# Kernel tuning notes

Hardware: AMD Instinct MI355X
Metric: run time of the kernel (lower is better)

The kernel has to match this reference:

```python
import jax, jax.numpy as jnp
import numpy as np

HID = 1024
HEADS = 16
HEAD_DIM = HID // HEADS
SCALE = np.sqrt(HEAD_DIM).astype(np.float32)


def setup_inputs() -> dict:
    key = jax.random.key(0)
    ks = jax.random.split(key, 13)
    B, S = 4, 2048
    inp = {
        'query': jax.random.normal(ks[0], (B, S, HID), jnp.float32),
        'key': jax.random.normal(ks[1], (B, S, HID), jnp.float32),
        'value': jax.random.normal(ks[2], (B, S, HID), jnp.float32),
        'mask': jax.random.randint(ks[3], (B, 1, 1, S), 0, 2, jnp.int32),
        'Wq': jax.random.normal(ks[4], (HID, HID), jnp.float32) / np.sqrt(HID),
        'bq': jax.random.normal(ks[5], (HID,), jnp.float32) * 0.02,
        'Wk': jax.random.normal(ks[6], (HID, HID), jnp.float32) / np.sqrt(HID),
        'bk': jax.random.normal(ks[7], (HID,), jnp.float32) * 0.02,
        'Wv': jax.random.normal(ks[8], (HID, HID), jnp.float32) / np.sqrt(HID),
        'bv': jax.random.normal(ks[9], (HID,), jnp.float32) * 0.02,
        'Wo': jax.random.normal(ks[10], (HID, HID), jnp.float32) / np.sqrt(HID),
        'bo': jax.random.normal(ks[11], (HID,), jnp.float32) * 0.02,
    }
    return inp


def reference(query, key, value, mask, Wq, bq, Wk, bk, Wv, bv, Wo, bo):
    B, Sq, _ = query.shape
    # nn.Linear: x @ W.T + b
    Q = (query @ Wq.T + bq).reshape(B, Sq, HEADS, HEAD_DIM)
    K = (key @ Wk.T + bk).reshape(B, -1, HEADS, HEAD_DIM)
    V = (value @ Wv.T + bv).reshape(B, -1, HEADS, HEAD_DIM)
    # energy: [B, H, Q, K]
    energy = jnp.einsum('bqnh,bknh->bnqk', Q, K) / SCALE
    energy = jnp.where(mask == 0, jnp.float32(-1e10), energy)
    attention = jax.nn.softmax(energy, axis=-1)  # dropout p=0.0 -> identity
    x = jnp.einsum('bnqk,bknh->bqnh', attention, V).reshape(B, Sq, HID)
    return x @ Wo.T + bo
```

## Files before the change

kernel.cpp:

```cpp
#include <hip/hip_runtime.h>
#include <cstddef>
#include <math.h>

#define S_LEN  2048
#define HID_C  1024
#define NHEADS 16
#define HDIM   64

typedef __attribute__((ext_vector_type(8))) short bf16x8;
typedef __attribute__((ext_vector_type(4))) float f32x4;
typedef __attribute__((ext_vector_type(16))) float f32x16;
typedef unsigned short ushort_t;

#define LOG2E 1.44269504088896f

__device__ __forceinline__ unsigned short f32_to_bf16_rn(float f) {
    unsigned int u = __float_as_uint(f);
    return (unsigned short)((u + 0x8000u) >> 16);
}

__device__ __forceinline__ float fexp2(float x) {
    float r;
    asm("v_exp_f32 %0, %1" : "=v"(r) : "v"(x));
    return r;
}

__device__ __forceinline__ void gload16(const ushort_t* g, ushort_t* l) {
    __builtin_amdgcn_global_load_lds(
        (const __attribute__((address_space(1))) void*)g,
        (__attribute__((address_space(3))) void*)l, 16, 0, 0);
}

__device__ __forceinline__ float tmax16(const f32x16& v) {
    float a0 = fmaxf(v[0], v[1]),   a1 = fmaxf(v[2], v[3]);
    float a2 = fmaxf(v[4], v[5]),   a3 = fmaxf(v[6], v[7]);
    float a4 = fmaxf(v[8], v[9]),   a5 = fmaxf(v[10], v[11]);
    float a6 = fmaxf(v[12], v[13]), a7 = fmaxf(v[14], v[15]);
    float b0 = fmaxf(a0, a1), b1 = fmaxf(a2, a3);
    float b2 = fmaxf(a4, a5), b3 = fmaxf(a6, a7);
    return fmaxf(fmaxf(b0, b1), fmaxf(b2, b3));
}
__device__ __forceinline__ float tsum16(const f32x16& v) {
    float a0 = v[0] + v[1],   a1 = v[2] + v[3];
    float a2 = v[4] + v[5],   a3 = v[6] + v[7];
    float a4 = v[8] + v[9],   a5 = v[10] + v[11];
    float a6 = v[12] + v[13], a7 = v[14] + v[15];
    float b0 = a0 + a1, b1 = a2 + a3, b2 = a4 + a5, b3 = a6 + a7;
    return (b0 + b1) + (b2 + b3);
}

__global__ void scan_mask(const int* __restrict__ mask, int* __restrict__ cidx,
                          int* __restrict__ nvalid, int* __restrict__ npads) {
    const int b = blockIdx.x;
    const int lane = threadIdx.x;
    int base = 0;
    for (int i = 0; i < S_LEN / 64; ++i) {
        const int s = i * 64 + lane;
        const int v = mask[b * S_LEN + s];
        const unsigned long long bal = __ballot(v != 0);
        const int pre = __popcll(bal & ((1ull << lane) - 1ull));
        if (v) cidx[b * S_LEN + base + pre] = s;
        base += (int)__popcll(bal);
    }
    if (lane == 0) { nvalid[b] = base; npads[b] = (base + 63) & ~63; }
}

#define CONVB 12288

__global__ void prep_gather(
    const float* __restrict__ query,
    const float* __restrict__ Wq, const float* __restrict__ Wk,
    const float* __restrict__ Wo, const float* __restrict__ Wv,
    const float* __restrict__ key, const float* __restrict__ value,
    const int* __restrict__ cidx, const int* __restrict__ nvalid,
    ushort_t* __restrict__ Qbf, ushort_t* __restrict__ Wqb,
    ushort_t* __restrict__ Wkb, ushort_t* __restrict__ Wob,
    ushort_t* __restrict__ Wvb,
    ushort_t* __restrict__ Kc, ushort_t* __restrict__ Vc,
    float* __restrict__ Mbc)
{
    if (blockIdx.x < CONVB) {
        const unsigned SEG = 4u * S_LEN * HID_C;
        const unsigned NW = HID_C * HID_C;
        unsigned i = (blockIdx.x * 256u + threadIdx.x) * 4u;
        const float* src; ushort_t* dst;
        if (i < SEG) { src = query; dst = Qbf; }
        else {
            i -= SEG;
            if (i < NW) { src = Wq; dst = Wqb; }
            else { i -= NW;
                if (i < NW) { src = Wk; dst = Wkb; }
                else { i -= NW;
                    if (i < NW) { src = Wo; dst = Wob; }
                    else { i -= NW; if (i >= NW) return; src = Wv; dst = Wvb; }
                }
            }
        }
        float4 v = *reinterpret_cast<const float4*>(src + i);
        uint2 p;
        p.x = ((unsigned)f32_to_bf16_rn(v.y) << 16) | f32_to_bf16_rn(v.x);
        p.y = ((unsigned)f32_to_bf16_rn(v.w) << 16) | f32_to_bf16_rn(v.z);
        *reinterpret_cast<uint2*>(dst + i) = p;
    } else {
        const int r = blockIdx.x - CONVB;
        const int b = r >> 11, j = r & 2047;
        const int tid = threadIdx.x;
        const int nv = nvalid[b];
        if (tid == 0) Mbc[r] = (j < nv) ? 0.f : -1e30f;
        const int np128 = (nv + 127) & ~127;
        if (j >= np128) return;
        uint2* kd = reinterpret_cast<uint2*>(Kc + (size_t)r * HID_C + tid * 4);
        uint2* vd = reinterpret_cast<uint2*>(Vc + (size_t)r * HID_C + tid * 4);
        if (j < nv) {
            const int src = cidx[b * S_LEN + j];
            const float4 kv = *reinterpret_cast<const float4*>(
                key + ((size_t)b * S_LEN + src) * HID_C + tid * 4);
            const float4 vv = *reinterpret_cast<const float4*>(
                value + ((size_t)b * S_LEN + src) * HID_C + tid * 4);
            uint2 kp, vp;
            kp.x = ((unsigned)f32_to_bf16_rn(kv.y) << 16) | f32_to_bf16_rn(kv.x);
            kp.y = ((unsigned)f32_to_bf16_rn(kv.w) << 16) | f32_to_bf16_rn(kv.z);
            vp.x = ((unsigned)f32_to_bf16_rn(vv.y) << 16) | f32_to_bf16_rn(vv.x);
            vp.y = ((unsigned)f32_to_bf16_rn(vv.w) << 16) | f32_to_bf16_rn(vv.z);
            *kd = kp; *vd = vp;
        } else {
            *kd = make_uint2(0u, 0u); *vd = make_uint2(0u, 0u);
        }
    }
}

__device__ __forceinline__ void gemm_core(
    const ushort_t* __restrict__ Ab, const ushort_t* __restrict__ Wb,
    const float* __restrict__ bias, ushort_t* __restrict__ outB,
    float* __restrict__ outF,
    int bm, int bn, int N, int K, float oscale, int omode,
    ushort_t* Ah, ushort_t* Bh)
{
    const int tid  = threadIdx.x;
    const int lane = tid & 63;
    const int wave = tid >> 6;
    const int wm = (wave >> 1) * 64;
    const int wn = (wave & 1) * 64;
    const int fr = lane & 15;
    const int kq = lane >> 4;

    int srow[2], skq[2];
#pragma unroll
    for (int i = 0; i < 2; ++i) {
        const int s = i * 256 + tid;
        srow[i] = s >> 2;
        skq[i] = (s & 3) ^ ((s >> 3) & 3);
    }
    const int wslot = tid & 192;

    f32x4 acc[4][4];
#pragma unroll
    for (int i = 0; i < 4; ++i)
#pragma unroll
        for (int j = 0; j < 4; ++j)
#pragma unroll
            for (int r = 0; r < 4; ++r) acc[i][j][r] = 0.f;

    for (int k0 = 0; k0 < K; k0 += 32) {
        __syncthreads();
#pragma unroll
        for (int i = 0; i < 2; ++i) {
            const int sb = (i * 256 + wslot) * 8;
            gload16(Ab + (size_t)(bm + srow[i]) * K + k0 + skq[i] * 8, Ah + sb);
            gload16(Wb + (size_t)(bn + srow[i]) * K + k0 + skq[i] * 8, Bh + sb);
        }
        __syncthreads();

        bf16x8 fah[4], fbh[4];
#pragma unroll
        for (int mi = 0; mi < 4; ++mi) {
            const int rr = wm + mi * 16 + fr;
            fah[mi] = *reinterpret_cast<const bf16x8*>(
                Ah + (rr * 4 + (kq ^ ((rr >> 1) & 3))) * 8);
        }
#pragma unroll
        for (int ni = 0; ni < 4; ++ni) {
            const int rr = wn + ni * 16 + fr;
            fbh[ni] = *reinterpret_cast<const bf16x8*>(
                Bh + (rr * 4 + (kq ^ ((rr >> 1) & 3))) * 8);
        }

#pragma unroll
        for (int mi = 0; mi < 4; ++mi)
#pragma unroll
            for (int ni = 0; ni < 4; ++ni)
                acc[mi][ni] = __builtin_amdgcn_mfma_f32_16x16x32_bf16(
                    fah[mi], fbh[ni], acc[mi][ni], 0, 0, 0);
    }

    const int fq = lane >> 4;
    if (omode == 2) {
#pragma unroll
        for (int mi = 0; mi < 4; ++mi)
#pragma unroll
            for (int r = 0; r < 4; ++r) {
                const int row = bm + wm + mi * 16 + fq * 4 + r;
                const float bvr = bias[row];
#pragma unroll
                for (int ni = 0; ni < 4; ++ni)
                    outB[(size_t)row * N + bn + wn + ni * 16 + fr] =
                        f32_to_bf16_rn((acc[mi][ni][r] + bvr) * oscale);
            }
    } else {
        float bv[4];
#pragma unroll
        for (int ni = 0; ni < 4; ++ni) bv[ni] = bias[bn + wn + ni * 16 + fr];
#pragma unroll
        for (int mi = 0; mi < 4; ++mi)
#pragma unroll
            for (int ni = 0; ni < 4; ++ni) {
                const size_t rowb = (size_t)(bm + wm + mi * 16 + fq * 4);
                const int col = bn + wn + ni * 16 + fr;
#pragma unroll
                for (int r = 0; r < 4; ++r) {
                    float v = (acc[mi][ni][r] + bv[ni]) * oscale;
                    if (omode == 0) outF[(rowb + r) * N + col] = v;
                    else            outB[(rowb + r) * N + col] = f32_to_bf16_rn(v);
                }
            }
    }
}

__global__ __launch_bounds__(256) void proj_fused(
    const ushort_t* __restrict__ Qbf, const ushort_t* __restrict__ Kc,
    const ushort_t* __restrict__ Wvb, const ushort_t* __restrict__ Vc,
    const ushort_t* __restrict__ Wqb, const ushort_t* __restrict__ Wkb,
    const float* __restrict__ bq, const float* __restrict__ bk,
    const float* __restrict__ bv, const int* __restrict__ npads,
    ushort_t* __restrict__ Qb, ushort_t* __restrict__ Kb,
    ushort_t* __restrict__ Vtg, float sc2)
{
    __shared__ __align__(16) ushort_t Ah[128 * 32];
    __shared__ __align__(16) ushort_t Bh[128 * 32];

    int id = blockIdx.x;
    if (id < 512) {
        const int bm = (((id >> 6) << 3) | (id & 7)) * 128;
        const int bn = ((id >> 3) & 7) * 128;
        gemm_core(Qbf, Wqb, bq, Qb, nullptr, bm, bn, HID_C, HID_C, sc2, 1, Ah, Bh);
    } else if (id < 1024) {
        id -= 512;
        const int bm = (((id >> 6) << 3) | (id & 7)) * 128;
        const int bn = ((id >> 3) & 7) * 128;
        if ((bm & 2047) >= npads[bm >> 11]) return;
        gemm_core(Kc, Wkb, bk, Kb, nullptr, bm, bn, HID_C, HID_C, 1.f, 1, Ah, Bh);
    } else {
        id -= 1024;
        const int bn = (id & 63) * 128;
        if ((bn & 2047) >= npads[bn >> 11]) return;
        gemm_core(Wvb, Vc, bv, Vtg, nullptr, (id >> 6) * 128, bn,
                  4 * S_LEN, HID_C, 1.f, 2, Ah, Bh);
    }
}

__global__ __launch_bounds__(256) void gemm_out(
    const ushort_t* __restrict__ Xb, const ushort_t* __restrict__ Wb,
    const float* __restrict__ bias, float* __restrict__ outF,
    int M, int N, int K)
{
    __shared__ __align__(16) ushort_t Ah[128 * 32];
    __shared__ __align__(16) ushort_t Bh[128 * 32];

    const int n = blockIdx.x;
    const int bm = ((((n >> 6) << 3) | (n & 7))) * 128;
    const int bn = ((n >> 3) & 7) * 128;
    gemm_core(Xb, Wb, bias, nullptr, outF, bm, bn, N, K, 1.f, 0, Ah, Bh);
}

#define QBLK 128
#define KVB  64
#define LDA  72

__global__ __launch_bounds__(256) void flash_attn_bf16(
    const ushort_t* __restrict__ Qb, const ushort_t* __restrict__ Kb,
    const ushort_t* __restrict__ Vtg, const float* __restrict__ maskb,
    const int* __restrict__ npads, ushort_t* __restrict__ Xb)
{
    __shared__ __align__(16) ushort_t Ks[KVB * LDA];
    __shared__ __align__(16) ushort_t Vt[HDIM * LDA];
    __shared__ float Xpose[QBLK];

    const int n  = blockIdx.x;
    const int bh = (n & 7) * 8 + ((n >> 3) & 7);
    const int qx = n >> 6;
    const int b  = bh >> 4;
    const int h  = bh & 15;
    const int q0 = qx * QBLK;

    const int tid  = threadIdx.x;
    const int lane = tid & 63;
    const int w    = tid >> 6;
    const int lq = lane & 31;
    const int lh = lane >> 5;

    const size_t bS = (size_t)b * S_LEN;
    const int hc = h * HDIM;
    const int npad = npads[b];

    bf16x8 qf[4];
#pragma unroll
    for (int s = 0; s < 4; ++s)
        qf[s] = *reinterpret_cast<const bf16x8*>(
            &Qb[(bS + q0 + w * 32 + lq) * HID_C + hc + s * 16 + lh * 8]);

    f32x16 OV[2], zc;
#pragma unroll
    for (int r = 0; r < 16; ++r) { OV[0][r] = 0.f; OV[1][r] = 0.f; zc[r] = 0.f; }
    float m_ = -1e30f, l_ = 0.f;

    const int sr  = tid >> 2;
    const int seg = tid & 3;
    const ushort_t* kbase = &Kb[(bS + sr) * HID_C + hc + seg * 16];
    const ushort_t* vbase = &Vtg[(size_t)(hc + sr) * (4 * S_LEN) + bS + seg * 16];

    {
        bf16x8 kv0 = *reinterpret_cast<const bf16x8*>(kbase);
        bf16x8 kv1 = *reinterpret_cast<const bf16x8*>(kbase + 8);
        bf16x8 vv0 = *reinterpret_cast<const bf16x8*>(vbase);
        bf16x8 vv1 = *reinterpret_cast<const bf16x8*>(vbase + 8);
        *reinterpret_cast<bf16x8*>(&Ks[sr * LDA + seg * 16])     = kv0;
        *reinterpret_cast<bf16x8*>(&Ks[sr * LDA + seg * 16 + 8]) = kv1;
        *reinterpret_cast<bf16x8*>(&Vt[sr * LDA + seg * 16])     = vv0;
        *reinterpret_cast<bf16x8*>(&Vt[sr * LDA + seg * 16 + 8]) = vv1;
        __syncthreads();
    }

    for (int t = 0; t < npad; t += KVB) {
        f32x16 S[2];
        __builtin_amdgcn_s_setprio(1);
#pragma unroll
        for (int kt = 0; kt < 2; ++kt) {
            bf16x8 kf0 = *reinterpret_cast<const bf16x8*>(
                &Ks[(kt * 32 + lq) * LDA + lh * 8]);
            S[kt] = __builtin_amdgcn_mfma_f32_32x32x16_bf16(kf0, qf[0], zc, 0, 0, 0);
#pragma unroll
            for (int s = 1; s < 4; ++s) {
                bf16x8 kf = *reinterpret_cast<const bf16x8*>(
                    &Ks[(kt * 32 + lq) * LDA + s * 16 + lh * 8]);
                S[kt] = __builtin_amdgcn_mfma_f32_32x32x16_bf16(
                    kf, qf[s], S[kt], 0, 0, 0);
            }
        }
        __builtin_amdgcn_s_setprio(0);

        const bool more = (t + KVB < npad);
        bf16x8 kv0n, kv1n, vv0n, vv1n;
        if (more) {
            const ushort_t* kp = kbase + (size_t)(t + KVB) * HID_C;
            const ushort_t* vp = vbase + (t + KVB);
            kv0n = *reinterpret_cast<const bf16x8*>(kp);
            kv1n = *reinterpret_cast<const bf16x8*>(kp + 8);
            vv0n = *reinterpret_cast<const bf16x8*>(vp);
            vv1n = *reinterpret_cast<const bf16x8*>(vp + 8);
        }

        if (!more) {
#pragma unroll
            for (int kt = 0; kt < 2; ++kt)
#pragma unroll
                for (int g = 0; g < 4; ++g) {
                    float4 mv = *reinterpret_cast<const float4*>(
                        &maskb[bS + t + kt * 32 + g * 8 + lh * 4]);
#pragma unroll
                    for (int e = 0; e < 4; ++e)
                        S[kt][g * 4 + e] += reinterpret_cast<const float*>(&mv)[e];
                }
        }

        float mx = fmaxf(tmax16(S[0]), tmax16(S[1]));
        mx = fmaxf(mx, __shfl_xor(mx, 32));

        if (!__all(mx <= m_ + 8.f)) {
            float mn = fmaxf(m_, mx);
            float corr = fexp2(m_ - mn);
            m_ = mn; l_ *= corr;
            if (lh == 0) Xpose[w * 32 + lq] = corr;
#pragma unroll
            for (int r = 0; r < 16; ++r) {
                float cq = Xpose[w * 32 + (r & 3) + 8 * (r >> 2) + 4 * lh];
                OV[0][r] *= cq;
                OV[1][r] *= cq;
            }
        }

#pragma unroll
        for (int kt = 0; kt < 2; ++kt)
#pragma unroll
            for (int r = 0; r < 16; ++r) S[kt][r] = fexp2(S[kt][r] - m_);
        float ls = tsum16(S[0]) + tsum16(S[1]);
        ls += __shfl_xor(ls, 32);
        l_ += ls;

        bf16x8 pa[4];
#pragma unroll
        for (int kt = 0; kt < 2; ++kt)
#pragma unroll
            for (int u = 0; u < 2; ++u) {
                const int bb = u * 8;
                unsigned int c0, c1, c2, c3;
                asm("v_cvt_pk_bf16_f32 %0, %1, %2"
                    : "=v"(c0) : "v"(S[kt][bb + 0]), "v"(S[kt][bb + 1]));
                asm("v_cvt_pk_bf16_f32 %0, %1, %2"
                    : "=v"(c1) : "v"(S[kt][bb + 2]), "v"(S[kt][bb + 3]));
                asm("v_cvt_pk_bf16_f32 %0, %1, %2"
                    : "=v"(c2) : "v"(S[kt][bb + 4]), "v"(S[kt][bb + 5]));
                asm("v_cvt_pk_bf16_f32 %0, %1, %2"
                    : "=v"(c3) : "v"(S[kt][bb + 6]), "v"(S[kt][bb + 7]));
                asm("v_permlane32_swap_b32 %0, %1" : "+v"(c0), "+v"(c2));
                asm("v_permlane32_swap_b32 %0, %1" : "+v"(c1), "+v"(c3));
                uint4 wv = make_uint4(c0, c1, c2, c3);
                pa[kt * 2 + u] = *reinterpret_cast<bf16x8*>(&wv);
            }

        __builtin_amdgcn_s_setprio(1);
#pragma unroll
        for (int dt = 0; dt < 2; ++dt)
#pragma unroll
            for (int f = 0; f < 4; ++f) {
                bf16x8 vf = *reinterpret_cast<const bf16x8*>(
                    &Vt[(dt * 32 + lq) * LDA + f * 16 + lh * 8]);
                OV[dt] = __builtin_amdgcn_mfma_f32_32x32x16_bf16(
                    pa[f], vf, OV[dt], 0, 0, 0);
            }
        __builtin_amdgcn_s_setprio(0);

        __syncthreads();
        if (more) {
            *reinterpret_cast<bf16x8*>(&Ks[sr * LDA + seg * 16])     = kv0n;
            *reinterpret_cast<bf16x8*>(&Ks[sr * LDA + seg * 16 + 8]) = kv1n;
            *reinterpret_cast<bf16x8*>(&Vt[sr * LDA + seg * 16])     = vv0n;
            *reinterpret_cast<bf16x8*>(&Vt[sr * LDA + seg * 16 + 8]) = vv1n;
            __syncthreads();
        }
    }

    if (lh == 0) Xpose[w * 32 + lq] = 1.f / l_;
#pragma unroll
    for (int r = 0; r < 16; ++r) {
        const int qr = (r & 3) + 8 * (r >> 2) + 4 * lh;
        const float inv = Xpose[w * 32 + qr];
        const size_t row = bS + q0 + w * 32 + qr;
#pragma unroll
        for (int dt = 0; dt < 2; ++dt)
            Xb[row * HID_C + hc + dt * 32 + lq] = f32_to_bf16_rn(OV[dt][r] * inv);
    }
}

extern "C" void kernel_launch(void* const* d_in, const int* in_sizes, int n_in,
                              void* d_out, int out_size, void* d_ws, size_t ws_size,
                              hipStream_t stream) {
    const float* query = (const float*)d_in[0];
    const float* key   = (const float*)d_in[1];
    const float* value = (const float*)d_in[2];
    const int*   mask  = (const int*)d_in[3];
    const float* Wq = (const float*)d_in[4];
    const float* bq = (const float*)d_in[5];
    const float* Wk = (const float*)d_in[6];
    const float* bk = (const float*)d_in[7];
    const float* Wv = (const float*)d_in[8];
    const float* bv = (const float*)d_in[9];
    const float* Wo = (const float*)d_in[10];
    const float* bo = (const float*)d_in[11];
    float* out = (float*)d_out;

    const int B = 4, M = B * S_LEN;
    const size_t seg = (size_t)M * HID_C;
    const size_t nw  = (size_t)HID_C * HID_C;

    ushort_t* Qb  = (ushort_t*)d_ws;
    ushort_t* Kb  = Qb + seg;
    ushort_t* Vtg = Kb + seg;
    ushort_t* Xb  = Vtg + seg;
    ushort_t* Vc  = Xb + seg;
    ushort_t* Qbf = Vc + seg;
    float*    Mbc = (float*)(Qbf + seg);
    ushort_t* Wqb = (ushort_t*)(Mbc + 4 * S_LEN);
    ushort_t* Wkb = Wqb + nw;
    ushort_t* Wob = Wkb + nw;
    ushort_t* Wvb = Wob + nw;
    int*      cidx   = (int*)(Wvb + nw);
    int*      nvalid = cidx + 4 * S_LEN;
    int*      npads  = nvalid + 4;

    ushort_t* Kc = Xb;

    scan_mask<<<dim3(4), 64, 0, stream>>>(mask, cidx, nvalid, npads);
    prep_gather<<<dim3(CONVB + M), 256, 0, stream>>>(
        query, Wq, Wk, Wo, Wv, key, value, cidx, nvalid,
        Qbf, Wqb, Wkb, Wob, Wvb, Kc, Vc, Mbc);

    const float SC2 = 0.125f * LOG2E;
    proj_fused<<<dim3(1536), 256, 0, stream>>>(
        Qbf, Kc, Wvb, Vc, Wqb, Wkb, bq, bk, bv, npads, Qb, Kb, Vtg, SC2);

    flash_attn_bf16<<<dim3((S_LEN / QBLK) * B * NHEADS), 256, 0, stream>>>(
        Qb, Kb, Vtg, Mbc, npads, Xb);

    gemm_out<<<dim3(512), 256, 0, stream>>>(
        Xb, Wob, bo, out, M, HID_C, HID_C);
}
```

Before: 180.6 us.

## Double the attention KV tile to 128 and drop register prefetch of next tile

The flash-attention kernel now processes 128 keys per iteration instead of 64, with the padded valid-key count rounded to 128. This halves the number of loop iterations, syncs and softmax rescale checks. The V tile gets its own padded stride, and the P-to-bf16 conversion is interleaved per 32-key chunk with the PV MFMAs. The register prefetch of the next K/V tile that overlapped the global loads with softmax is removed: loads now happen after the barrier, unhidden, and more padding work is done for masked keys.

```diff
diff --git a/kernel.cpp b/kernel.cpp
--- a/kernel.cpp
+++ b/kernel.cpp
@@ -62,7 +62,7 @@
         if (v) cidx[b * S_LEN + base + pre] = s;
         base += (int)__popcll(bal);
     }
-    if (lane == 0) { nvalid[b] = base; npads[b] = (base + 63) & ~63; }
+    if (lane == 0) { nvalid[b] = base; npads[b] = (base + 127) & ~127; }
 }
 
 #define CONVB 12288
@@ -273,16 +273,17 @@
 }
 
 #define QBLK 128
-#define KVB  64
+#define KVB  128
 #define LDA  72
-
-__global__ __launch_bounds__(256) void flash_attn_bf16(
+#define LDV  136
+
+__global__ __launch_bounds__(256, 4) void flash_attn_bf16(
     const ushort_t* __restrict__ Qb, const ushort_t* __restrict__ Kb,
     const ushort_t* __restrict__ Vtg, const float* __restrict__ maskb,
     const int* __restrict__ npads, ushort_t* __restrict__ Xb)
 {
     __shared__ __align__(16) ushort_t Ks[KVB * LDA];
-    __shared__ __align__(16) ushort_t Vt[HDIM * LDA];
+    __shared__ __align__(16) ushort_t Vt[HDIM * LDV];
     __shared__ float Xpose[QBLK];
 
     const int n  = blockIdx.x;
@@ -313,28 +314,29 @@
     for (int r = 0; r < 16; ++r) { OV[0][r] = 0.f; OV[1][r] = 0.f; zc[r] = 0.f; }
     float m_ = -1e30f, l_ = 0.f;
 
-    const int sr  = tid >> 2;
-    const int seg = tid & 3;
-    const ushort_t* kbase = &Kb[(bS + sr) * HID_C + hc + seg * 16];
-    const ushort_t* vbase = &Vtg[(size_t)(hc + sr) * (4 * S_LEN) + bS + seg * 16];
+    const int sr = tid >> 1, sc = (tid & 1) * 32;
+    const int vr = tid >> 2, vc = (tid & 3) * 32;
+    const ushort_t* kbase = &Kb[(bS + sr) * HID_C + hc + sc];
+    const ushort_t* vbase = &Vtg[(size_t)(hc + vr) * (4 * S_LEN) + bS + vc];
 
     {
-        bf16x8 kv0 = *reinterpret_cast<const bf16x8*>(kbase);
-        bf16x8 kv1 = *reinterpret_cast<const bf16x8*>(kbase + 8);
-        bf16x8 vv0 = *reinterpret_cast<const bf16x8*>(vbase);
-        bf16x8 vv1 = *reinterpret_cast<const bf16x8*>(vbase + 8);
-        *reinterpret_cast<bf16x8*>(&Ks[sr * LDA + seg * 16])     = kv0;
-        *reinterpret_cast<bf16x8*>(&Ks[sr * LDA + seg * 16 + 8]) = kv1;
-        *reinterpret_cast<bf16x8*>(&Vt[sr * LDA + seg * 16])     = vv0;
-        *reinterpret_cast<bf16x8*>(&Vt[sr * LDA + seg * 16 + 8]) = vv1;
+#pragma unroll
+        for (int c = 0; c < 4; ++c) {
+            bf16x8 kv = *reinterpret_cast<const bf16x8*>(kbase + c * 8);
+            *reinterpret_cast<bf16x8*>(&Ks[sr * LDA + sc + c * 8]) = kv;
+            bf16x8 vv = *reinterpret_cast<const bf16x8*>(vbase + c * 8);
+            *reinterpret_cast<bf16x8*>(&Vt[vr * LDV + vc + c * 8]) = vv;
+        }
         __syncthreads();
     }
 
     for (int t = 0; t < npad; t += KVB) {
-        f32x16 S[2];
+        const bool more = (t + KVB < npad);
+
+        f32x16 S[4];
         __builtin_amdgcn_s_setprio(1);
 #pragma unroll
-        for (int kt = 0; kt < 2; ++kt) {
+        for (int kt = 0; kt < 4; ++kt) {
             bf16x8 kf0 = *reinterpret_cast<const bf16x8*>(
                 &Ks[(kt * 32 + lq) * LDA + lh * 8]);
             S[kt] = __builtin_amdgcn_mfma_f32_32x32x16_bf16(kf0, qf[0], zc, 0, 0, 0);
@@ -348,20 +350,9 @@
         }
         __builtin_amdgcn_s_setprio(0);
 
-        const bool more = (t + KVB < npad);
-        bf16x8 kv0n, kv1n, vv0n, vv1n;
-        if (more) {
-            const ushort_t* kp = kbase + (size_t)(t + KVB) * HID_C;
-            const ushort_t* vp = vbase + (t + KVB);
-            kv0n = *reinterpret_cast<const bf16x8*>(kp);
-            kv1n = *reinterpret_cast<const bf16x8*>(kp + 8);
-            vv0n = *reinterpret_cast<const bf16x8*>(vp);
-            vv1n = *reinterpret_cast<const bf16x8*>(vp + 8);
-        }
-
         if (!more) {
 #pragma unroll
-            for (int kt = 0; kt < 2; ++kt)
+            for (int kt = 0; kt < 4; ++kt)
 #pragma unroll
                 for (int g = 0; g < 4; ++g) {
                     float4 mv = *reinterpret_cast<const float4*>(
@@ -372,7 +363,8 @@
                 }
         }
 
-        float mx = fmaxf(tmax16(S[0]), tmax16(S[1]));
+        float mx = fmaxf(fmaxf(tmax16(S[0]), tmax16(S[1])),
+                         fmaxf(tmax16(S[2]), tmax16(S[3])));
         mx = fmaxf(mx, __shfl_xor(mx, 32));
 
         if (!__all(mx <= m_ + 8.f)) {
@@ -389,16 +381,17 @@
         }
 
 #pragma unroll
-        for (int kt = 0; kt < 2; ++kt)
+        for (int kt = 0; kt < 4; ++kt)
 #pragma unroll
             for (int r = 0; r < 16; ++r) S[kt][r] = fexp2(S[kt][r] - m_);
-        float ls = tsum16(S[0]) + tsum16(S[1]);
+        float ls = (tsum16(S[0]) + tsum16(S[1])) + (tsum16(S[2]) + tsum16(S[3]));
         ls += __shfl_xor(ls, 32);
         l_ += ls;
 
-        bf16x8 pa[4];
-#pragma unroll
-        for (int kt = 0; kt < 2; ++kt)
+        __builtin_amdgcn_s_setprio(1);
+#pragma unroll
+        for (int kt = 0; kt < 4; ++kt) {
+            bf16x8 pa[2];
 #pragma unroll
             for (int u = 0; u < 2; ++u) {
                 const int bb = u * 8;
@@ -414,29 +407,33 @@
                 asm("v_permlane32_swap_b32 %0, %1" : "+v"(c0), "+v"(c2));
                 asm("v_permlane32_swap_b32 %0, %1" : "+v"(c1), "+v"(c3));
                 uint4 wv = make_uint4(c0, c1, c2, c3);
-                pa[kt * 2 + u] = *reinterpret_cast<bf16x8*>(&wv);
+                pa[u] = *reinterpret_cast<bf16x8*>(&wv);
             }
-
-        __builtin_amdgcn_s_setprio(1);
-#pragma unroll
-        for (int dt = 0; dt < 2; ++dt)
-#pragma unroll
-            for (int f = 0; f < 4; ++f) {
-                bf16x8 vf = *reinterpret_cast<const bf16x8*>(
-                    &Vt[(dt * 32 + lq) * LDA + f * 16 + lh * 8]);
-                OV[dt] = __builtin_amdgcn_mfma_f32_32x32x16_bf16(
-                    pa[f], vf, OV[dt], 0, 0, 0);
-            }
+#pragma unroll
+            for (int dt = 0; dt < 2; ++dt)
+#pragma unroll
+                for (int u = 0; u < 2; ++u) {
+                    bf16x8 vf = *reinterpret_cast<const bf16x8*>(
+                        &Vt[(dt * 32 + lq) * LDV + (kt * 2 + u) * 16 + lh * 8]);
+                    OV[dt] = __builtin_amdgcn_mfma_f32_32x32x16_bf16(
+                        pa[u], vf, OV[dt], 0, 0, 0);
+                }
+        }
         __builtin_amdgcn_s_setprio(0);
 
+        if (!more) break;
+
         __syncthreads();
-        if (more) {
-            *reinterpret_cast<bf16x8*>(&Ks[sr * LDA + seg * 16])     = kv0n;
-            *reinterpret_cast<bf16x8*>(&Ks[sr * LDA + seg * 16 + 8]) = kv1n;
-            *reinterpret_cast<bf16x8*>(&Vt[sr * LDA + seg * 16])     = vv0n;
-            *reinterpret_cast<bf16x8*>(&Vt[sr * LDA + seg * 16 + 8]) = vv1n;
-            __syncthreads();
-        }
+#pragma unroll
+        for (int c = 0; c < 4; ++c) {
+            bf16x8 kv = *reinterpret_cast<const bf16x8*>(
+                kbase + (size_t)(t + KVB) * HID_C + c * 8);
+            *reinterpret_cast<bf16x8*>(&Ks[sr * LDA + sc + c * 8]) = kv;
+            bf16x8 vv = *reinterpret_cast<const bf16x8*>(
+                vbase + (t + KVB) + c * 8);
+            *reinterpret_cast<bf16x8*>(&Vt[vr * LDV + vc + c * 8]) = vv;
+        }
+        __syncthreads();
     }
 
     if (lh == 0) Xpose[w * 32 + lq] = 1.f / l_;
```

After: 235.4 us. 30.4% more time.
